# Kernel optimization log

Measured on AMD Instinct MI355X. Metric: run time of the kernel, lower is better.

## Reference

```python
import jax, jax.numpy as jnp
import numpy as np

T, Hs, Ws, MAX_D = 8, 14, 14, 3
D_WIN = 2 * MAX_D + 1  # 7


def l2norm(x, axis, eps=1e-12):
    # matches torch F.normalize
    n = jnp.sqrt(jnp.sum(x * x, axis=axis, keepdims=True))
    return x / jnp.maximum(n, eps)


def correlation(q, k):
    # q, k: (B, d, H, W). FlowNet-style cost volume with max_displacement=3,
    # kernel_size=1, zero padding at borders. Output (B, 49, H*W).
    B, d, H, W = q.shape
    kp = jnp.pad(k, ((0, 0), (0, 0), (MAX_D, MAX_D), (MAX_D, MAX_D)))
    planes = [jnp.sum(q * kp[:, :, u:u + H, v:v + W], axis=1)
              for u in range(D_WIN) for v in range(D_WIN)]
    return jnp.stack(planes, axis=1).reshape(B, D_WIN * D_WIN, H * W)


def setup_inputs() -> dict:
    key = jax.random.key(0)
    ks = jax.random.split(key, 5)
    B, N, C = 16, T * Hs * Ws, 768
    x = jax.random.normal(ks[0], (B, N, C), dtype=jnp.float32)
    w_qkv = jax.random.normal(ks[1], (C, 3 * C), dtype=jnp.float32) * (1.0 / np.sqrt(C))
    w_proj = jax.random.normal(ks[2], (C, C), dtype=jnp.float32) * (1.0 / np.sqrt(C))
    b_proj = jnp.zeros((C,), dtype=jnp.float32)
    pos_embed = jax.random.normal(ks[3], (1, D_WIN * D_WIN, Hs * Ws), dtype=jnp.float32) * 0.02
    return {"x": x, "w_qkv": w_qkv, "w_proj": w_proj, "b_proj": b_proj,
            "pos_embed": pos_embed}


def reference(x, w_qkv, w_proj, b_proj, pos_embed):
    B, N, C = x.shape
    nh = 8
    hd = C // nh
    HW = Hs * Ws
    # qkv: (3, B, nh, N, hd)
    qkv = (x @ w_qkv).reshape(B, N, 3, nh, hd).transpose(2, 0, 3, 1, 4)
    q, k, v = qkv[0], qkv[1], qkv[2]
    # 'b n (t h w) d -> (b n) t d h w'
    q = q.reshape(B * nh, T, Hs, Ws, hd).transpose(0, 1, 4, 2, 3)
    k = k.reshape(B * nh, T, Hs, Ws, hd).transpose(0, 1, 4, 2, 3)
    # v: '(b n t) (h w) d'
    v = v.reshape(B * nh * T, HW, hd)
    # temporal shift: k_postfix[t] = k[t+1], last repeated
    k_post = jnp.concatenate([k[:, 1:], k[:, -1:]], axis=1)
    qp = l2norm(q.reshape(B * nh * T, hd, Hs, Ws), axis=1)
    kp = l2norm(k_post.reshape(B * nh * T, hd, Hs, Ws), axis=1)
    # cost volume (BhT, 49, HW) + positional embedding
    corr = correlation(qp, kp) + pos_embed
    # motion branch: corr^T @ corr -> (BhT, HW, HW)
    motion_attn = jax.nn.softmax(jnp.einsum('bun,bum->bnm', corr, corr), axis=-1)
    motion_x = jnp.einsum('bnm,bmd->bnd', motion_attn, v)
    # appearance branch
    qf = qp.reshape(B * nh * T, hd, HW).transpose(0, 2, 1)  # (BhT, HW, hd)
    kf = kp.reshape(B * nh * T, hd, HW)                      # (BhT, hd, HW)
    app_attn = jax.nn.softmax(jnp.einsum('bnd,bdm->bnm', qf, kf), axis=-1)
    app_x = jnp.einsum('bnm,bmd->bnd', app_attn, v)

    def merge(y):
        # '(b n t) (h w) d -> b n (t h w) d' then 'b h n d -> b n (h d)'
        y = y.reshape(B, nh, T * HW, hd).transpose(0, 2, 1, 3)
        return y.reshape(B, N, C)

    out = 0.5 * merge(app_x) + 0.5 * merge(motion_x)
    return out @ w_proj + b_proj
```

## Files before the change

### kernel.cpp

```cpp
#include <hip/hip_runtime.h>
#include <hip/hip_bf16.h>

namespace {

constexpr int T = 8, HW = 196;
constexpr int C = 768, NH = 8, HD = 96;
constexpr int NTOK = 1568;
constexpr int BHT = 1024;
constexpr int C3 = 2304;
constexpr int CHW = HD * HW;
constexpr int NROWS = 25088;
constexpr int NT = 13;
constexpr int KW = 104;
constexpr int VW2 = 212;
constexpr int UW = 72;
constexpr int TSZ = 128 * 64;

using bf16 = __hip_bfloat16;
typedef __attribute__((ext_vector_type(8))) short short8v;
typedef __attribute__((ext_vector_type(4))) float f32x4;

__device__ __forceinline__ float b2f(bf16 h) { return __bfloat162float(h); }
__device__ __forceinline__ bf16 f2b(float f) { return __float2bfloat16(f); }
__device__ __forceinline__ float u2f(ushort u) {
  union { ushort u[2]; float f; } x; x.u[0] = 0; x.u[1] = u; return x.f;
}
__device__ __forceinline__ ushort b2u(bf16 h) { union { bf16 b; ushort u; } x; x.b = h; return x.u; }
__device__ __forceinline__ uint pk2(float lo, float hi) {
  return ((uint)b2u(f2b(hi)) << 16) | (uint)b2u(f2b(lo));
}
__device__ __forceinline__ void gload_lds16(const bf16* g, bf16* l) {
  __builtin_amdgcn_global_load_lds(
      (const __attribute__((address_space(1))) unsigned int*)g,
      (__attribute__((address_space(3))) unsigned int*)l, 16, 0, 0);
}

__global__ __launch_bounds__(256) void conv_to_bf16(
    const float* __restrict__ X, bf16* __restrict__ Y, int n8) {
  const int i = blockIdx.x * 256 + threadIdx.x;
  if (i >= n8) return;
  const float4 a = ((const float4*)X)[i * 2];
  const float4 b = ((const float4*)X)[i * 2 + 1];
  uint4 o;
  o.x = pk2(a.x, a.y); o.y = pk2(a.z, a.w);
  o.z = pk2(b.x, b.y); o.w = pk2(b.z, b.w);
  ((uint4*)Y)[i] = o;
}

__global__ __launch_bounds__(256) void transpose_to_bf16(
    const float* __restrict__ W, bf16* __restrict__ Wt, int rows, int cols) {
  __shared__ __align__(16) bf16 Lt[64][72];
  const int r0 = blockIdx.y * 64, c0 = blockIdx.x * 64;
  const int tid = threadIdx.x;
  const int r = tid >> 2, q = (tid & 3) * 16;
  const float* src = W + (size_t)(r0 + r) * cols + c0 + q;
#pragma unroll
  for (int i = 0; i < 16; i += 4) {
    const float4 v = *(const float4*)(src + i);
    Lt[q + i + 0][r] = f2b(v.x);
    Lt[q + i + 1][r] = f2b(v.y);
    Lt[q + i + 2][r] = f2b(v.z);
    Lt[q + i + 3][r] = f2b(v.w);
  }
  __syncthreads();
  const int c = tid >> 2, kc = (tid & 3) * 16;
  uint4* dst = (uint4*)(Wt + (size_t)(c0 + c) * rows + r0 + kc);
  const uint4* srcl = (const uint4*)(&Lt[c][kc]);
  dst[0] = srcl[0];
  dst[1] = srcl[1];
}

__device__ __forceinline__ void gemm128_core(
    const bf16* __restrict__ A, const bf16* __restrict__ Bt,
    int rt, int ct, bf16* As, bf16* Bs, f32x4 acc[4][4]) {
  const int tid = threadIdx.x;
  const int w = tid >> 6, lane = tid & 63;
  const int lr = lane & 15, lg = lane >> 4;
  const int wr = w >> 1, wc = w & 1;
  const int crow = (lane >> 3);
  const int cole = ((lane & 7) ^ crow) << 3;
#pragma unroll
  for (int i = 0; i < 4; ++i)
#pragma unroll
    for (int j = 0; j < 4; ++j) acc[i][j] = (f32x4){0.f, 0.f, 0.f, 0.f};

  for (int kt = 0; kt < 12; ++kt) {
    const int k0 = kt * 64;
    __syncthreads();
#pragma unroll
    for (int i = 0; i < 4; ++i) {
      const int chunk = w * 4 + i;
      const int row = chunk * 8 + crow;
      gload_lds16(A + (size_t)(rt + row) * 768 + k0 + cole, As + chunk * 512);
      gload_lds16(Bt + (size_t)(ct + row) * 768 + k0 + cole, Bs + chunk * 512);
    }
    __syncthreads();
#pragma unroll
    for (int kc = 0; kc < 2; ++kc) {
      const int roff = ((kc * 4 + lg) ^ (lr & 7)) << 3;
      short8v xa[4], wb[4];
#pragma unroll
      for (int f = 0; f < 4; ++f) {
        xa[f] = *(const short8v*)(As + (wr * 64 + f * 16 + lr) * 64 + roff);
        wb[f] = *(const short8v*)(Bs + (wc * 64 + f * 16 + lr) * 64 + roff);
      }
#pragma unroll
      for (int cj = 0; cj < 4; ++cj)
#pragma unroll
        for (int ri = 0; ri < 4; ++ri)
          acc[cj][ri] = __builtin_amdgcn_mfma_f32_16x16x32_bf16(wb[cj], xa[ri], acc[cj][ri], 0, 0, 0);
    }
  }
}

__global__ __launch_bounds__(256, 3) void gemm_qkv_mfma(
    const bf16* __restrict__ A, const bf16* __restrict__ Bt,
    bf16* __restrict__ Qo, bf16* __restrict__ Ko, bf16* __restrict__ Vo) {
  __shared__ __align__(16) bf16 As[TSZ];
  __shared__ __align__(16) bf16 Bs[TSZ];
  const int id = blockIdx.x;
  const int sw = (id & 7) * 441 + (id >> 3);
  const int cti = sw % 18, rti = sw / 18;
  const int ct = cti * 128, rt = rti * 128;
  const int tid = threadIdx.x;
  const int w = tid >> 6, lane = tid & 63;
  const int lr = lane & 15, lg = lane >> 4;
  const int wr = w >> 1, wc = w & 1;

  f32x4 acc[4][4];
  gemm128_core(A, Bt, rt, ct, As, Bs, acc);

  const int s = cti / 6;
#pragma unroll
  for (int ri = 0; ri < 4; ++ri) {
    const int row = rt + wr * 64 + ri * 16 + lr;
    const int b_ = row / NTOK, n = row % NTOK;
    const int t = n / HW, hw = n % HW;
#pragma unroll
    for (int cj = 0; cj < 4; ++cj) {
      const int colb = ct + wc * 64 + cj * 16 + lg * 4;
      const int rem = colb - s * C;
      const int head = rem / HD, chb = rem - head * HD;
      const int bh = b_ * NH + head;
      if (s == 0) {
        uint2 pk;
        pk.x = pk2(acc[cj][ri][0], acc[cj][ri][1]);
        pk.y = pk2(acc[cj][ri][2], acc[cj][ri][3]);
        *(uint2*)(Qo + (size_t)(bh * T + t) * CHW + hw * HD + chb) = pk;
      } else if (s == 1) {
        uint2 pk;
        pk.x = pk2(acc[cj][ri][0], acc[cj][ri][1]);
        pk.y = pk2(acc[cj][ri][2], acc[cj][ri][3]);
        if (t >= 1)
          *(uint2*)(Ko + (size_t)(bh * T + t - 1) * CHW + hw * HD + chb) = pk;
        if (t == T - 1)
          *(uint2*)(Ko + (size_t)(bh * T + t) * CHW + hw * HD + chb) = pk;
      } else {
#pragma unroll
        for (int j = 0; j < 4; ++j)
          Vo[(size_t)(bh * T + t) * CHW + (chb + j) * HW + hw] = f2b(acc[cj][ri][j]);
      }
    }
  }
}

__global__ __launch_bounds__(256, 3) void gemm_proj_mfma(
    const bf16* __restrict__ A, const bf16* __restrict__ Bt,
    const float* __restrict__ bias, float* __restrict__ out) {
  __shared__ __align__(16) bf16 As[TSZ];
  __shared__ __align__(16) bf16 Bs[TSZ];
  const int id = blockIdx.x;
  const int sw = (id & 7) * 147 + (id >> 3);
  const int cti = sw % 6, rti = sw / 6;
  const int ct = cti * 128, rt = rti * 128;
  const int tid = threadIdx.x;
  const int w = tid >> 6, lane = tid & 63;
  const int lr = lane & 15, lg = lane >> 4;
  const int wr = w >> 1, wc = w & 1;

  f32x4 acc[4][4];
  gemm128_core(A, Bt, rt, ct, As, Bs, acc);

#pragma unroll
  for (int ri = 0; ri < 4; ++ri) {
    const int row = rt + wr * 64 + ri * 16 + lr;
#pragma unroll
    for (int cj = 0; cj < 4; ++cj) {
      const int colb = ct + wc * 64 + cj * 16 + lg * 4;
      const float4 bv = *(const float4*)(bias + colb);
      float4 o;
      o.x = acc[cj][ri][0] + bv.x;
      o.y = acc[cj][ri][1] + bv.y;
      o.z = acc[cj][ri][2] + bv.z;
      o.w = acc[cj][ri][3] + bv.w;
      *(float4*)(out + (size_t)row * C + colb) = o;
    }
  }
}

__global__ __launch_bounds__(1024, 1) void fused_attn(
    const bf16* __restrict__ Qg, const bf16* __restrict__ Kg,
    const bf16* __restrict__ Vg, const float* __restrict__ pos,
    bf16* __restrict__ merged) {
  __shared__ __align__(16) bf16 Klds[208 * KW];
  __shared__ __align__(16) bf16 Vt[96 * VW2];
  __shared__ __align__(16) bf16 corrT[208 * UW];
  __shared__ float invQ[208];
  const int bt = blockIdx.x;
  const int tid = threadIdx.x;
  const int w = tid >> 6, lane = tid & 63;
  const int lr = lane & 15, lg = lane >> 4;
  const size_t gbase = (size_t)bt * CHW;

  {
    const uint4* kg = (const uint4*)(Kg + gbase);
    uint4* kl = (uint4*)Klds;
    for (int i = tid; i < 196 * 12; i += 1024) { const int r = i / 12, g = i - r * 12; kl[r * 13 + g] = kg[i]; }
    const uint4 z4 = make_uint4(0u, 0u, 0u, 0u);
    for (int i = tid; i < 12 * 13; i += 1024) { const int r = 196 + i / 13, g = i % 13; kl[r * 13 + g] = z4; }
    const uint* vg = (const uint*)(Vg + gbase);
    uint* vl = (uint*)Vt;
    for (int i = tid; i < 96 * 98; i += 1024) { const int c = i / 98, g = i - c * 98; vl[c * 106 + g] = vg[i]; }
    for (int i = tid; i < 96 * 8; i += 1024)  { const int c = i / 8, g = 98 + (i & 7); vl[c * 106 + g] = 0u; }
    uint* ct32 = (uint*)corrT;
    for (int i = tid; i < 208 * 36; i += 1024) {
      const int n = i % 208, up = i / 208;
      const int u0 = 2 * up, u1 = u0 + 1;
      const float p0 = (n < 196 && u0 < 49) ? pos[u0 * 196 + n] : 0.f;
      const float p1 = (n < 196 && u1 < 49) ? pos[u1 * 196 + n] : 0.f;
      ct32[n * 36 + up] = pk2(p0, p1);
    }
    if (tid < 208) {
      float s = 0.f;
      if (tid < 196) {
        const uint* qr = (const uint*)(Qg + gbase + (size_t)tid * HD);
#pragma unroll
        for (int g = 0; g < 48; ++g) {
          const uint pk = qr[g];
          const float a = u2f((ushort)(pk & 0xffff));
          const float b = u2f((ushort)(pk >> 16));
          s += a * a + b * b;
        }
      }
      invQ[tid] = 1.f / fmaxf(sqrtf(s), 1e-12f);
    }
  }
  __syncthreads();
  if (tid < 208) {
    uint* rowp = (uint*)(Klds + tid * KW);
    float s = 0.f;
#pragma unroll
    for (int g = 0; g < 48; ++g) {
      const uint pk = rowp[g];
      const float a = u2f((ushort)(pk & 0xffff));
      const float b = u2f((ushort)(pk >> 16));
      s += a * a + b * b;
    }
    const float inv = 1.f / fmaxf(sqrtf(s), 1e-12f);
#pragma unroll
    for (int g = 0; g < 48; ++g) {
      const uint pk = rowp[g];
      rowp[g] = pk2(u2f((ushort)(pk & 0xffff)) * inv, u2f((ushort)(pk >> 16)) * inv);
    }
  }
  __syncthreads();

  const int b_ = bt >> 6, head = (bt >> 3) & 7, tt = bt & 7;
  union PW { short8v v; uint u[4]; };
  const int rt = w;
  f32x4 pacc[6];
#pragma unroll
  for (int ct = 0; ct < 6; ++ct) pacc[ct] = (f32x4){0.f, 0.f, 0.f, 0.f};

  if (rt < NT) {
    const int rq = (rt * 16 + lr > 195) ? 195 : rt * 16 + lr;
    short8v qf[3];
#pragma unroll
    for (int kc = 0; kc < 3; ++kc)
      qf[kc] = *(const short8v*)(Qg + gbase + (size_t)rq * HD + kc * 32 + lg * 8);
    f32x4 sacc[NT];
#pragma unroll
    for (int mt = 0; mt < NT; ++mt) sacc[mt] = (f32x4){0.f, 0.f, 0.f, 0.f};
    __builtin_amdgcn_s_setprio(1);
#pragma unroll
    for (int kc = 0; kc < 3; ++kc)
#pragma unroll
      for (int mt = 0; mt < NT; ++mt) {
        const short8v kf = *(const short8v*)&Klds[(mt * 16 + lr) * KW + kc * 32 + lg * 8];
        sacc[mt] = __builtin_amdgcn_mfma_f32_16x16x32_bf16(kf, qf[kc], sacc[mt], 0, 0, 0);
      }
    __builtin_amdgcn_s_setprio(0);
    const float iq = invQ[rq];
#pragma unroll
    for (int mt = 0; mt < NT; ++mt) {
      sacc[mt][0] *= iq; sacc[mt][1] *= iq; sacc[mt][2] *= iq; sacc[mt][3] *= iq;
    }
    const int rowg = rt * 16 + lr;
    if (rowg < 196) {
      const int h = rowg / 14, wq = rowg - (rowg / 14) * 14;
      int h2 = 0, w2 = lg * 4;
#pragma unroll
      for (int mt = 0; mt < NT; ++mt) {
        int hh = h2, ww = w2;
#pragma unroll
        for (int r = 0; r < 4; ++r) {
          if (mt < 12 || lg * 4 + r < 4) {
            const int dh = hh - h + 3, dw = ww - wq + 3;
            if (((unsigned)dh < 7u) && ((unsigned)dw < 7u)) {
              bf16* cp = &corrT[rowg * UW + dh * 7 + dw];
              *cp = f2b(b2f(*cp) + sacc[mt][r]);
            }
          }
          if (++ww == 14) { ww = 0; ++hh; }
        }
        w2 += 2; h2 += 1; if (w2 >= 14) { w2 -= 14; h2 += 1; }
      }
    }
    float m0 = -1e30f, m1 = -1e30f, m2 = -1e30f, m3 = -1e30f;
#pragma unroll
    for (int mt = 0; mt < 12; ++mt) {
      m0 = fmaxf(m0, sacc[mt][0]); m1 = fmaxf(m1, sacc[mt][1]);
      m2 = fmaxf(m2, sacc[mt][2]); m3 = fmaxf(m3, sacc[mt][3]);
    }
    if (lg == 0) {
      m0 = fmaxf(m0, sacc[12][0]); m1 = fmaxf(m1, sacc[12][1]);
      m2 = fmaxf(m2, sacc[12][2]); m3 = fmaxf(m3, sacc[12][3]);
    }
    float mx = fmaxf(fmaxf(m0, m1), fmaxf(m2, m3));
    mx = fmaxf(mx, __shfl_xor(mx, 16));
    mx = fmaxf(mx, __shfl_xor(mx, 32));
    float s0 = 0.f, s1 = 0.f, s2 = 0.f, s3 = 0.f;
#pragma unroll
    for (int mt = 0; mt < NT; ++mt) {
      const bool dead = (mt == 12) && (lg != 0);
      const float e0 = dead ? 0.f : __expf(sacc[mt][0] - mx);
      const float e1 = dead ? 0.f : __expf(sacc[mt][1] - mx);
      const float e2 = dead ? 0.f : __expf(sacc[mt][2] - mx);
      const float e3 = dead ? 0.f : __expf(sacc[mt][3] - mx);
      sacc[mt][0] = e0; sacc[mt][1] = e1; sacc[mt][2] = e2; sacc[mt][3] = e3;
      s0 += e0; s1 += e1; s2 += e2; s3 += e3;
    }
    float s = (s0 + s1) + (s2 + s3);
    s += __shfl_xor(s, 16); s += __shfl_xor(s, 32);
    const float sc = 0.5f / s;
    PW pf[7];
#pragma unroll
    for (int kb = 0; kb < 7; ++kb) {
      pf[kb].u[0] = pk2(sacc[2 * kb][0] * sc, sacc[2 * kb][1] * sc);
      pf[kb].u[1] = pk2(sacc[2 * kb][2] * sc, sacc[2 * kb][3] * sc);
      if (kb < 6) {
        pf[kb].u[2] = pk2(sacc[2 * kb + 1][0] * sc, sacc[2 * kb + 1][1] * sc);
        pf[kb].u[3] = pk2(sacc[2 * kb + 1][2] * sc, sacc[2 * kb + 1][3] * sc);
      } else { pf[kb].u[2] = 0u; pf[kb].u[3] = 0u; }
    }
    __builtin_amdgcn_s_setprio(1);
#pragma unroll
    for (int ct = 0; ct < 6; ++ct) {
      const int c = ct * 16 + lr;
#pragma unroll
      for (int kb = 0; kb < 7; ++kb) {
        const uint2 lo = *(const uint2*)&Vt[c * VW2 + (2 * kb) * 16 + lg * 4];
        const uint2 hi = (kb < 6) ? *(const uint2*)&Vt[c * VW2 + (2 * kb + 1) * 16 + lg * 4] : lo;
        PW vf; vf.u[0] = lo.x; vf.u[1] = lo.y; vf.u[2] = hi.x; vf.u[3] = hi.y;
        pacc[ct] = __builtin_amdgcn_mfma_f32_16x16x32_bf16(pf[kb].v, vf.v, pacc[ct], 0, 0, 0);
      }
    }
    __builtin_amdgcn_s_setprio(0);
  }
  __syncthreads();

  if (rt < NT) {
    short8v cq[2];
#pragma unroll
    for (int kc = 0; kc < 2; ++kc)
      cq[kc] = *(const short8v*)&corrT[(rt * 16 + lr) * UW + kc * 32 + lg * 8];
    f32x4 macc[NT];
#pragma unroll
    for (int mt = 0; mt < NT; ++mt) macc[mt] = (f32x4){0.f, 0.f, 0.f, 0.f};
    __builtin_amdgcn_s_setprio(1);
#pragma unroll
    for (int kc = 0; kc < 2; ++kc)
#pragma unroll
      for (int mt = 0; mt < NT; ++mt) {
        const short8v ca = *(const short8v*)&corrT[(mt * 16 + lr) * UW + kc * 32 + lg * 8];
        macc[mt] = __builtin_amdgcn_mfma_f32_16x16x32_bf16(ca, cq[kc], macc[mt], 0, 0, 0);
      }
    __builtin_amdgcn_s_setprio(0);
    float m0 = -1e30f, m1 = -1e30f, m2 = -1e30f, m3 = -1e30f;
#pragma unroll
    for (int mt = 0; mt < 12; ++mt) {
      m0 = fmaxf(m0, macc[mt][0]); m1 = fmaxf(m1, macc[mt][1]);
      m2 = fmaxf(m2, macc[mt][2]); m3 = fmaxf(m3, macc[mt][3]);
    }
    if (lg == 0) {
      m0 = fmaxf(m0, macc[12][0]); m1 = fmaxf(m1, macc[12][1]);
      m2 = fmaxf(m2, macc[12][2]); m3 = fmaxf(m3, macc[12][3]);
    }
    float mx = fmaxf(fmaxf(m0, m1), fmaxf(m2, m3));
    mx = fmaxf(mx, __shfl_xor(mx, 16));
    mx = fmaxf(mx, __shfl_xor(mx, 32));
    float s0 = 0.f, s1 = 0.f, s2 = 0.f, s3 = 0.f;
#pragma unroll
    for (int mt = 0; mt < NT; ++mt) {
      const bool dead = (mt == 12) && (lg != 0);
      const float e0 = dead ? 0.f : __expf(macc[mt][0] - mx);
      const float e1 = dead ? 0.f : __expf(macc[mt][1] - mx);
      const float e2 = dead ? 0.f : __expf(macc[mt][2] - mx);
      const float e3 = dead ? 0.f : __expf(macc[mt][3] - mx);
      macc[mt][0] = e0; macc[mt][1] = e1; macc[mt][2] = e2; macc[mt][3] = e3;
      s0 += e0; s1 += e1; s2 += e2; s3 += e3;
    }
    float s = (s0 + s1) + (s2 + s3);
    s += __shfl_xor(s, 16); s += __shfl_xor(s, 32);
    const float sc = 0.5f / s;
    PW pf[7];
#pragma unroll
    for (int kb = 0; kb < 7; ++kb) {
      pf[kb].u[0] = pk2(macc[2 * kb][0] * sc, macc[2 * kb][1] * sc);
      pf[kb].u[1] = pk2(macc[2 * kb][2] * sc, macc[2 * kb][3] * sc);
      if (kb < 6) {
        pf[kb].u[2] = pk2(macc[2 * kb + 1][0] * sc, macc[2 * kb + 1][1] * sc);
        pf[kb].u[3] = pk2(macc[2 * kb + 1][2] * sc, macc[2 * kb + 1][3] * sc);
      } else { pf[kb].u[2] = 0u; pf[kb].u[3] = 0u; }
    }
    __builtin_amdgcn_s_setprio(1);
#pragma unroll
    for (int ct = 0; ct < 6; ++ct) {
      const int c = ct * 16 + lr;
#pragma unroll
      for (int kb = 0; kb < 7; ++kb) {
        const uint2 lo = *(const uint2*)&Vt[c * VW2 + (2 * kb) * 16 + lg * 4];
        const uint2 hi = (kb < 6) ? *(const uint2*)&Vt[c * VW2 + (2 * kb + 1) * 16 + lg * 4] : lo;
        PW vf; vf.u[0] = lo.x; vf.u[1] = lo.y; vf.u[2] = hi.x; vf.u[3] = hi.y;
        pacc[ct] = __builtin_amdgcn_mfma_f32_16x16x32_bf16(pf[kb].v, vf.v, pacc[ct], 0, 0, 0);
      }
    }
    __builtin_amdgcn_s_setprio(0);
#pragma unroll
    for (int r = 0; r < 4; ++r) {
      const int rowq = rt * 16 + lg * 4 + r;
      if (rowq < 196) {
        const size_t ob = ((size_t)(b_ * NTOK + tt * HW + rowq)) * C + head * HD;
#pragma unroll
        for (int ct = 0; ct < 6; ++ct)
          merged[ob + ct * 16 + lr] = f2b(pacc[ct][r]);
      }
    }
  }
}

}

extern "C" void kernel_launch(void* const* d_in, const int* in_sizes, int n_in,
                              void* d_out, int out_size, void* d_ws, size_t ws_size,
                              hipStream_t stream) {
  (void)in_sizes; (void)n_in; (void)out_size; (void)ws_size;
  const float* x      = (const float*)d_in[0];
  const float* w_qkv  = (const float*)d_in[1];
  const float* w_proj = (const float*)d_in[2];
  const float* b_proj = (const float*)d_in[3];
  const float* pos    = (const float*)d_in[4];
  float* out = (float*)d_out;

  char* p = (char*)d_ws;
  bf16* Qb = (bf16*)p;      p += (size_t)BHT * CHW * sizeof(bf16);
  bf16* Kb = (bf16*)p;      p += (size_t)BHT * CHW * sizeof(bf16);
  bf16* Vb = (bf16*)p;      p += (size_t)BHT * CHW * sizeof(bf16);
  bf16* xbm = (bf16*)p;     p += (size_t)NROWS * C * sizeof(bf16);
  bf16* wqkvT = (bf16*)p;   p += (size_t)C3 * C * sizeof(bf16);
  bf16* wprojT = (bf16*)p;  p += (size_t)C * C * sizeof(bf16);

  conv_to_bf16<<<(NROWS * C / 8 + 255) / 256, 256, 0, stream>>>(x, xbm, NROWS * C / 8);
  transpose_to_bf16<<<dim3(C3 / 64, C / 64), 256, 0, stream>>>(w_qkv, wqkvT, C, C3);
  transpose_to_bf16<<<dim3(C / 64, C / 64), 256, 0, stream>>>(w_proj, wprojT, C, C);
  gemm_qkv_mfma<<<3528, 256, 0, stream>>>(xbm, wqkvT, Qb, Kb, Vb);
  fused_attn<<<BHT, 1024, 0, stream>>>(Qb, Kb, Vb, pos, xbm );
  gemm_proj_mfma<<<1176, 256, 0, stream>>>(xbm, wprojT, b_proj, out);
}
```

Before: 295.9 us.

## Swizzle corrT LDS layout, defer pos-embed add, and parallelize row norms

Shrinks the correlation tile in LDS to 64-wide rows with an XOR swizzle on 8-element groups, which should reduce bank conflicts on the MFMA fragment reads. The positional embedding is no longer preloaded into corrT. It is added in a separate pass after the scatter, so the scatter becomes a plain store instead of a read-modify-write. The Q and K L2-norm computations now spread each row across 4 threads with shuffle reductions instead of one thread per row. This adds an extra barrier and pass over corrT, and the index math must stay consistent across the writer and both readers.

```diff
diff --git a/kernel.cpp b/kernel.cpp
--- a/kernel.cpp
+++ b/kernel.cpp
@@ -13,7 +13,6 @@
 constexpr int NT = 13;
 constexpr int KW = 104;
 constexpr int VW2 = 212;
-constexpr int UW = 72;
 constexpr int TSZ = 128 * 64;
 
 using bf16 = __hip_bfloat16;
@@ -204,7 +203,7 @@
     bf16* __restrict__ merged) {
   __shared__ __align__(16) bf16 Klds[208 * KW];
   __shared__ __align__(16) bf16 Vt[96 * VW2];
-  __shared__ __align__(16) bf16 corrT[208 * UW];
+  __shared__ __align__(16) bf16 corrT[208 * 64];
   __shared__ float invQ[208];
   const int bt = blockIdx.x;
   const int tid = threadIdx.x;
@@ -222,43 +221,45 @@
     uint* vl = (uint*)Vt;
     for (int i = tid; i < 96 * 98; i += 1024) { const int c = i / 98, g = i - c * 98; vl[c * 106 + g] = vg[i]; }
     for (int i = tid; i < 96 * 8; i += 1024)  { const int c = i / 8, g = 98 + (i & 7); vl[c * 106 + g] = 0u; }
-    uint* ct32 = (uint*)corrT;
-    for (int i = tid; i < 208 * 36; i += 1024) {
-      const int n = i % 208, up = i / 208;
-      const int u0 = 2 * up, u1 = u0 + 1;
-      const float p0 = (n < 196 && u0 < 49) ? pos[u0 * 196 + n] : 0.f;
-      const float p1 = (n < 196 && u1 < 49) ? pos[u1 * 196 + n] : 0.f;
-      ct32[n * 36 + up] = pk2(p0, p1);
-    }
-    if (tid < 208) {
+    uint4* cz = (uint4*)corrT;
+    for (int i = tid; i < 1664; i += 1024) cz[i] = z4;
+    if (tid < 832) {
+      const int row = tid >> 2, sub = tid & 3;
       float s = 0.f;
-      if (tid < 196) {
-        const uint* qr = (const uint*)(Qg + gbase + (size_t)tid * HD);
-#pragma unroll
-        for (int g = 0; g < 48; ++g) {
-          const uint pk = qr[g];
-          const float a = u2f((ushort)(pk & 0xffff));
-          const float b = u2f((ushort)(pk >> 16));
-          s += a * a + b * b;
+      if (row < 196) {
+        const uint4* qr = (const uint4*)(Qg + gbase + (size_t)row * HD) + sub * 3;
+#pragma unroll
+        for (int g = 0; g < 3; ++g) {
+          const uint4 v = qr[g];
+          const uint uu[4] = {v.x, v.y, v.z, v.w};
+#pragma unroll
+          for (int q = 0; q < 4; ++q) {
+            const float a = u2f((ushort)(uu[q] & 0xffff));
+            const float b = u2f((ushort)(uu[q] >> 16));
+            s += a * a + b * b;
+          }
         }
       }
-      invQ[tid] = 1.f / fmaxf(sqrtf(s), 1e-12f);
+      s += __shfl_xor(s, 1); s += __shfl_xor(s, 2);
+      if (sub == 0) invQ[row] = 1.f / fmaxf(sqrtf(s), 1e-12f);
     }
   }
   __syncthreads();
-  if (tid < 208) {
-    uint* rowp = (uint*)(Klds + tid * KW);
+  if (tid < 832) {
+    const int row = tid >> 2, sub = tid & 3;
+    uint* rowp = (uint*)(Klds + row * KW) + sub * 12;
     float s = 0.f;
 #pragma unroll
-    for (int g = 0; g < 48; ++g) {
+    for (int g = 0; g < 12; ++g) {
       const uint pk = rowp[g];
       const float a = u2f((ushort)(pk & 0xffff));
       const float b = u2f((ushort)(pk >> 16));
       s += a * a + b * b;
     }
+    s += __shfl_xor(s, 1); s += __shfl_xor(s, 2);
     const float inv = 1.f / fmaxf(sqrtf(s), 1e-12f);
 #pragma unroll
-    for (int g = 0; g < 48; ++g) {
+    for (int g = 0; g < 12; ++g) {
       const uint pk = rowp[g];
       rowp[g] = pk2(u2f((ushort)(pk & 0xffff)) * inv, u2f((ushort)(pk >> 16)) * inv);
     }
@@ -298,6 +299,8 @@
     const int rowg = rt * 16 + lr;
     if (rowg < 196) {
       const int h = rowg / 14, wq = rowg - (rowg / 14) * 14;
+      bf16* crow = corrT + rowg * 64;
+      const int rsw = rowg & 7;
       int h2 = 0, w2 = lg * 4;
 #pragma unroll
       for (int mt = 0; mt < NT; ++mt) {
@@ -307,8 +310,8 @@
           if (mt < 12 || lg * 4 + r < 4) {
             const int dh = hh - h + 3, dw = ww - wq + 3;
             if (((unsigned)dh < 7u) && ((unsigned)dw < 7u)) {
-              bf16* cp = &corrT[rowg * UW + dh * 7 + dw];
-              *cp = f2b(b2f(*cp) + sacc[mt][r]);
+              const int u = dh * 7 + dw;
+              crow[(((u >> 3) ^ rsw) << 3) + (u & 7)] = f2b(sacc[mt][r]);
             }
           }
           if (++ww == 14) { ww = 0; ++hh; }
@@ -369,11 +372,28 @@
   }
   __syncthreads();
 
+  {
+    uint* ct32 = (uint*)corrT;
+    for (int i = tid; i < 208 * 25; i += 1024) {
+      const int n = i % 208, wp = i / 208;
+      if (n < 196) {
+        const int u0 = 2 * wp, u1 = u0 + 1;
+        const int ad = n * 32 + (((wp >> 2) ^ (n & 7)) << 2) + (wp & 3);
+        const uint pk = ct32[ad];
+        const float v0 = u2f((ushort)(pk & 0xffff)) + pos[u0 * 196 + n];
+        const float v1 = u2f((ushort)(pk >> 16)) + (u1 < 49 ? pos[u1 * 196 + n] : 0.f);
+        ct32[ad] = pk2(v0, v1);
+      }
+    }
+  }
+  __syncthreads();
+
   if (rt < NT) {
+    const int csw = lr & 7;
     short8v cq[2];
 #pragma unroll
     for (int kc = 0; kc < 2; ++kc)
-      cq[kc] = *(const short8v*)&corrT[(rt * 16 + lr) * UW + kc * 32 + lg * 8];
+      cq[kc] = *(const short8v*)&corrT[(rt * 16 + lr) * 64 + (((kc * 4 + lg) ^ csw) << 3)];
     f32x4 macc[NT];
 #pragma unroll
     for (int mt = 0; mt < NT; ++mt) macc[mt] = (f32x4){0.f, 0.f, 0.f, 0.f};
@@ -382,7 +402,7 @@
     for (int kc = 0; kc < 2; ++kc)
 #pragma unroll
       for (int mt = 0; mt < NT; ++mt) {
-        const short8v ca = *(const short8v*)&corrT[(mt * 16 + lr) * UW + kc * 32 + lg * 8];
+        const short8v ca = *(const short8v*)&corrT[(mt * 16 + lr) * 64 + (((kc * 4 + lg) ^ csw) << 3)];
         macc[mt] = __builtin_amdgcn_mfma_f32_16x16x32_bf16(ca, cq[kc], macc[mt], 0, 0, 0);
       }
     __builtin_amdgcn_s_setprio(0);
```

After: 286.0 us. 3.3% less time.
